# Performance work log

Hardware: AMD Instinct MI355X
Metric: run time of the kernel (lower is better)

## Reference

```python
import jax, jax.numpy as jnp
import numpy as np

B, C_IN, H, W = 4, 128, 56, 56
G = 4            # num_groups
K = 3            # kernel_size
PAD = 1
STRIDE = 1
NG = 8           # grid_size (num RBF centers)
GRID_MIN, GRID_MAX = -1.0, 1.0
C_OUT = 128
CG = C_IN // G           # 32 channels per group
D = CG * K * K           # 288 per-group patch dim
OG = C_OUT // G          # 32 outputs per group


def setup_inputs() -> dict:
    key = jax.random.key(0)
    k1, k2, k3, k4 = jax.random.split(key, 4)
    x = jax.random.normal(k1, (B, C_IN, H, W), dtype=jnp.float32)
    spline_w = jax.random.normal(k2, (G, OG, D * NG), dtype=jnp.float32) * (1.0 / np.sqrt(D * NG))
    base_w = jax.random.normal(k3, (G, OG, D), dtype=jnp.float32) * (1.0 / np.sqrt(D))
    base_b = jax.random.normal(k4, (G, OG), dtype=jnp.float32) * 0.01
    return {"x": x, "spline_w": spline_w, "base_w": base_w, "base_b": base_b}


def _im2col(x):
    # x: (B, C, H, W) -> patches (B, C*K*K, Ho, Wo), unfold ordering (c, kh, kw)
    xp = jnp.pad(x, ((0, 0), (0, 0), (PAD, PAD), (PAD, PAD)))
    Ho = (H + 2 * PAD - K) // STRIDE + 1
    Wo = (W + 2 * PAD - K) // STRIDE + 1
    # fixed 3x3 loop over kernel offsets (9 slices), vectorized over B,C,H,W
    shards = [xp[:, :, i:i + Ho, j:j + Wo] for i in range(K) for j in range(K)]
    p = jnp.stack(shards, axis=2)             # (B, C, K*K, Ho, Wo)
    return p.reshape(x.shape[0], -1, Ho, Wo)  # (B, C*K*K, Ho, Wo)


def reference(x, spline_w, base_w, base_b):
    Ho = (H + 2 * PAD - K) // STRIDE + 1
    Wo = (W + 2 * PAD - K) // STRIDE + 1
    L = Ho * Wo
    patches = _im2col(x)                                   # (B, C*9, Ho, Wo)
    # groups are contiguous channel blocks -> split channel-major patch dim
    p = patches.reshape(B, G, D, L).transpose(0, 1, 3, 2)  # (B, G, L, D)
    # RBF spline basis: exp(-((x - c)/h)^2)
    grid = jnp.linspace(GRID_MIN, GRID_MAX, NG, dtype=p.dtype)   # (NG,)
    h = (GRID_MAX - GRID_MIN) / (NG - 1)
    basis = jnp.exp(-(((p[..., None] - grid) / h) ** 2))         # (B, G, L, D, NG)
    basis = basis.reshape(B, G, L, D * NG)
    spline_out = jnp.einsum('bgld,god->bglo', basis, spline_w)   # (B, G, L, OG)
    base_out = jnp.einsum('bgld,god->bglo', jax.nn.silu(p), base_w) + base_b[None, :, None, :]
    out = spline_out + base_out                                  # (B, G, L, OG)
    # torch.cat(group outs, dim=1) -> per-pixel channel order is group-major
    out = out.transpose(0, 2, 1, 3).reshape(B, L, G * OG)        # (B, L, C_OUT)
    out = out.transpose(0, 2, 1).reshape(B, C_OUT, Ho, Wo)
    return out
```

## Files before the change

kernel.cpp:

```cpp
#include <hip/hip_runtime.h>

#define BATCH 4
#define C_IN 128
#define HWD 56
#define L_PIX 3136
#define G_GRP 4
#define CG 32
#define D_DIM 288
#define NG 8
#define OG 32
#define NQ_SPL 72
#define NQ_BASE 9
#define LOG2E 1.44269504f

typedef short  short8 __attribute__((ext_vector_type(8)));
typedef float  f32x4  __attribute__((ext_vector_type(4)));

__device__ __forceinline__ short f2bf(float f) {
    __bf16 h = (__bf16)f;
    return __builtin_bit_cast(short, h);
}

__global__ __launch_bounds__(256) void convert_w_kernel(
    const float* __restrict__ spline_w,
    const float* __restrict__ base_w,
    short* __restrict__ wspl,
    short* __restrict__ wbase)
{
    int t = blockIdx.x * 256 + threadIdx.x;
    if (t >= G_GRP * (NQ_SPL + NQ_BASE) * 2 * 64) return;
    int lane = t & 63;
    int rest = t >> 6;
    int ot = rest & 1;
    int gq = rest >> 1;
    int g  = gq / (NQ_SPL + NQ_BASE);
    int q  = gq - g * (NQ_SPL + NQ_BASE);
    int o  = ot * 16 + (lane & 15);
    int dl = lane >> 4;
    if (q < NQ_SPL) {
        int d = 4 * q + dl;
        const float* src = spline_w + (size_t)(g * OG + o) * (D_DIM * NG) + d * NG;
        short* dst = wspl + ((size_t)((g * NQ_SPL + q) * 2 + ot) * 64 + lane) * 8;
#pragma unroll
        for (int j = 0; j < 8; ++j) dst[j] = f2bf(src[j]);
    } else {
        int qb = q - NQ_SPL;
        int d0 = qb * 32 + dl * 8;
        const float* src = base_w + (size_t)(g * OG + o) * D_DIM + d0;
        short* dst = wbase + ((size_t)((g * NQ_BASE + qb) * 2 + ot) * 64 + lane) * 8;
#pragma unroll
        for (int j = 0; j < 8; ++j) dst[j] = f2bf(src[j]);
    }
}

__global__ __launch_bounds__(256, 3) void groupkan_mfma_kernel(
    const float* __restrict__ x,
    const float* __restrict__ base_b,
    const short* __restrict__ wspl,
    const short* __restrict__ wbase,
    float* __restrict__ out)
{
    __shared__ float xt[CG][4][58];

    const int tid  = threadIdx.x;
    const int tile = blockIdx.x;
    const int bg   = blockIdx.y;
    const int b = bg >> 2, g = bg & 3;
    const int l0 = tile * 64;
    const int y0 = l0 / HWD;

    const float* xg = x + (size_t)(b * C_IN + g * CG) * L_PIX;
    for (int e = tid; e < CG * 4 * 58; e += 256) {
        int c  = e / 232;
        int r  = e - c * 232;
        int ry = r / 58;
        int rx = r - ry * 58;
        int y  = y0 - 1 + ry;
        int xc = rx - 1;
        float v = 0.0f;
        if (y >= 0 && y < HWD && xc >= 0 && xc < HWD)
            v = xg[(size_t)c * L_PIX + y * HWD + xc];
        xt[c][ry][rx] = v;
    }
    __syncthreads();

    const int lane = tid & 63;
    const int wid  = tid >> 6;
    const int fr   = lane & 15;
    const int dl   = lane >> 4;
    const int l    = l0 + wid * 16 + fr;
    const int yy   = l / HWD;
    const int xx   = l - yy * HWD;
    const int ybase = yy - y0;

    f32x4 acc0, acc1;
    {
        float b0 = base_b[g * OG + fr];
        float b1 = base_b[g * OG + 16 + fr];
        acc0 = (f32x4){b0, b0, b0, b0};
        acc1 = (f32x4){b1, b1, b1, b1};
    }

    const short8* wspg = (const short8*)wspl + (size_t)g * NQ_SPL * 2 * 64;
    const short8* wbg  = (const short8*)wbase + (size_t)g * NQ_BASE * 2 * 64;

    int c = 0, kk = dl;
    for (int q = 0; q < NQ_SPL; ++q) {
        int kh = (kk * 11) >> 5;
        int kw = kk - kh * 3;
        float v = xt[c][ybase + kh][xx + kw];
        float v35p = v * 3.5f + 3.5f;
        short8 a;
#pragma unroll
        for (int j = 0; j < 8; ++j) {
            float u = v35p - (float)j;
            float e = __builtin_amdgcn_exp2f(u * u * (-LOG2E));
            a[j] = f2bf(e);
        }
        short8 bf0 = wspg[(q * 2 + 0) * 64 + lane];
        short8 bf1 = wspg[(q * 2 + 1) * 64 + lane];
        acc0 = __builtin_amdgcn_mfma_f32_16x16x32_bf16(a, bf0, acc0, 0, 0, 0);
        acc1 = __builtin_amdgcn_mfma_f32_16x16x32_bf16(a, bf1, acc1, 0, 0, 0);
        kk += 4; if (kk >= 9) { kk -= 9; ++c; }
    }

    for (int q = 0; q < NQ_BASE; ++q) {
        int d0 = q * 32 + dl * 8;
        int cc = (d0 * 456) >> 12;
        int kb = d0 - cc * 9;
        short8 a;
#pragma unroll
        for (int j = 0; j < 8; ++j) {
            int kh = (kb * 11) >> 5;
            int kw = kb - kh * 3;
            float v = xt[cc][ybase + kh][xx + kw];
            float ex = __builtin_amdgcn_exp2f(v * (-LOG2E));
            float s  = v * __builtin_amdgcn_rcpf(1.0f + ex);
            a[j] = f2bf(s);
            ++kb; if (kb == 9) { kb = 0; ++cc; }
        }
        short8 bf0 = wbg[(q * 2 + 0) * 64 + lane];
        short8 bf1 = wbg[(q * 2 + 1) * 64 + lane];
        acc0 = __builtin_amdgcn_mfma_f32_16x16x32_bf16(a, bf0, acc0, 0, 0, 0);
        acc1 = __builtin_amdgcn_mfma_f32_16x16x32_bf16(a, bf1, acc1, 0, 0, 0);
    }

    float* outp = out + (size_t)(b * C_IN + g * OG) * L_PIX;
    int pix = l0 + wid * 16 + dl * 4;
    *(f32x4*)(outp + (size_t)fr * L_PIX + pix)        = acc0;
    *(f32x4*)(outp + (size_t)(16 + fr) * L_PIX + pix) = acc1;
}

extern "C" void kernel_launch(void* const* d_in, const int* in_sizes, int n_in,
                              void* d_out, int out_size, void* d_ws, size_t ws_size,
                              hipStream_t stream) {
    const float* x        = (const float*)d_in[0];
    const float* spline_w = (const float*)d_in[1];
    const float* base_w   = (const float*)d_in[2];
    const float* base_b   = (const float*)d_in[3];
    float* out = (float*)d_out;

    short* wspl  = (short*)d_ws;
    short* wbase = wspl + (size_t)G_GRP * NQ_SPL * 2 * 64 * 8;

    int conv_threads = G_GRP * (NQ_SPL + NQ_BASE) * 2 * 64;
    convert_w_kernel<<<(conv_threads + 255) / 256, 256, 0, stream>>>(
        spline_w, base_w, wspl, wbase);

    dim3 grid(L_PIX / 64, BATCH * G_GRP);
    groupkan_mfma_kernel<<<grid, 256, 0, stream>>>(x, base_b, wspl, wbase, out);
}
```

Before: 114.5 us.

## Reassign reduction dim per lane, fold RBF scaling into exp2, vectorize weight conversion

```diff
diff --git a/kernel.cpp b/kernel.cpp
--- a/kernel.cpp
+++ b/kernel.cpp
@@ -12,14 +12,21 @@
 #define NQ_SPL 72
 #define NQ_BASE 9
 #define LOG2E 1.44269504f
+#define SQRT_L 1.2011224087f
+#define A_SCL  4.2039284306f
 
 typedef short  short8 __attribute__((ext_vector_type(8)));
 typedef float  f32x4  __attribute__((ext_vector_type(4)));
-
-__device__ __forceinline__ short f2bf(float f) {
-    __bf16 h = (__bf16)f;
-    return __builtin_bit_cast(short, h);
-}
+typedef unsigned int u32x4 __attribute__((ext_vector_type(4)));
+
+__device__ __forceinline__ unsigned int pack2(float lo, float hi) {
+    unsigned short a = __builtin_bit_cast(unsigned short, (__bf16)lo);
+    unsigned short b = __builtin_bit_cast(unsigned short, (__bf16)hi);
+    return (unsigned int)a | ((unsigned int)b << 16);
+}
+
+#define N_SPL_CHUNK (G_GRP * OG * D_DIM)
+#define N_BASE_CHUNK (G_GRP * OG * D_DIM / 8)
 
 __global__ __launch_bounds__(256) void convert_w_kernel(
     const float* __restrict__ spline_w,
@@ -28,28 +35,42 @@
     short* __restrict__ wbase)
 {
     int t = blockIdx.x * 256 + threadIdx.x;
-    if (t >= G_GRP * (NQ_SPL + NQ_BASE) * 2 * 64) return;
-    int lane = t & 63;
-    int rest = t >> 6;
-    int ot = rest & 1;
-    int gq = rest >> 1;
-    int g  = gq / (NQ_SPL + NQ_BASE);
-    int q  = gq - g * (NQ_SPL + NQ_BASE);
-    int o  = ot * 16 + (lane & 15);
-    int dl = lane >> 4;
-    if (q < NQ_SPL) {
-        int d = 4 * q + dl;
-        const float* src = spline_w + (size_t)(g * OG + o) * (D_DIM * NG) + d * NG;
-        short* dst = wspl + ((size_t)((g * NQ_SPL + q) * 2 + ot) * 64 + lane) * 8;
-#pragma unroll
-        for (int j = 0; j < 8; ++j) dst[j] = f2bf(src[j]);
+    if (t >= N_SPL_CHUNK + N_BASE_CHUNK) return;
+    if (t < N_SPL_CHUNK) {
+        const f32x4* s4 = (const f32x4*)spline_w + (size_t)t * 2;
+        f32x4 lo = s4[0], hi = s4[1];
+        int flat = t * 8;
+        int g = flat / (OG * D_DIM * NG);
+        int r = flat - g * (OG * D_DIM * NG);
+        int o = r / (D_DIM * NG);
+        int d = (r - o * (D_DIM * NG)) >> 3;
+        int dl = d / 72;
+        int q  = d - dl * 72;
+        int lane = dl * 16 + (o & 15);
+        int ot = o >> 4;
+        u32x4 pk;
+        pk.x = pack2(lo.x, lo.y); pk.y = pack2(lo.z, lo.w);
+        pk.z = pack2(hi.x, hi.y); pk.w = pack2(hi.z, hi.w);
+        u32x4* dst = (u32x4*)wspl + (((size_t)(g * NQ_SPL + q) * 2 + ot) * 64 + lane);
+        *dst = pk;
     } else {
-        int qb = q - NQ_SPL;
-        int d0 = qb * 32 + dl * 8;
-        const float* src = base_w + (size_t)(g * OG + o) * D_DIM + d0;
-        short* dst = wbase + ((size_t)((g * NQ_BASE + qb) * 2 + ot) * 64 + lane) * 8;
-#pragma unroll
-        for (int j = 0; j < 8; ++j) dst[j] = f2bf(src[j]);
+        int tb = t - N_SPL_CHUNK;
+        const f32x4* s4 = (const f32x4*)base_w + (size_t)tb * 2;
+        f32x4 lo = s4[0], hi = s4[1];
+        int flat = tb * 8;
+        int g = flat / (OG * D_DIM);
+        int r = flat - g * (OG * D_DIM);
+        int o = r / D_DIM;
+        int d0 = r - o * D_DIM;
+        int dl = d0 / 72;
+        int q  = (d0 - dl * 72) >> 3;
+        int lane = dl * 16 + (o & 15);
+        int ot = o >> 4;
+        u32x4 pk;
+        pk.x = pack2(lo.x, lo.y); pk.y = pack2(lo.z, lo.w);
+        pk.z = pack2(hi.x, hi.y); pk.w = pack2(hi.z, hi.w);
+        u32x4* dst = (u32x4*)wbase + (((size_t)(g * NQ_BASE + q) * 2 + ot) * 64 + lane);
+        *dst = pk;
     }
 }
 
@@ -93,6 +114,8 @@
     const int xx   = l - yy * HWD;
     const int ybase = yy - y0;
 
+    const float* P = (const float*)xt + (dl * 8) * 232 + ybase * 58 + xx;
+
     f32x4 acc0, acc1;
     {
         float b0 = base_b[g * OG + fr];
@@ -101,46 +124,61 @@
         acc1 = (f32x4){b1, b1, b1, b1};
     }
 
-    const short8* wspg = (const short8*)wspl + (size_t)g * NQ_SPL * 2 * 64;
-    const short8* wbg  = (const short8*)wbase + (size_t)g * NQ_BASE * 2 * 64;
-
-    int c = 0, kk = dl;
-    for (int q = 0; q < NQ_SPL; ++q) {
-        int kh = (kk * 11) >> 5;
-        int kw = kk - kh * 3;
-        float v = xt[c][ybase + kh][xx + kw];
-        float v35p = v * 3.5f + 3.5f;
-        short8 a;
+    const short8* wl  = (const short8*)wspl + (size_t)g * NQ_SPL * 2 * 64 + lane;
+    const short8* wbl = (const short8*)wbase + (size_t)g * NQ_BASE * 2 * 64 + lane;
+
+    for (int qo = 0; qo < 8; ++qo) {
+        const float* Pc = P + qo * 232;
+#pragma unroll
+        for (int qi = 0; qi < 9; ++qi) {
+            const int kh = qi / 3, kw = qi % 3;
+            float v  = Pc[kh * 58 + kw];
+            float ap = v * A_SCL + A_SCL;
+            float e0, e1, e2, e3, e4, e5, e6, e7;
+            {
+                float u;
+                u = ap - 0.0f * SQRT_L; e0 = __builtin_amdgcn_exp2f(-(u * u));
+                u = ap - 1.0f * SQRT_L; e1 = __builtin_amdgcn_exp2f(-(u * u));
+                u = ap - 2.0f * SQRT_L; e2 = __builtin_amdgcn_exp2f(-(u * u));
+                u = ap - 3.0f * SQRT_L; e3 = __builtin_amdgcn_exp2f(-(u * u));
+                u = ap - 4.0f * SQRT_L; e4 = __builtin_amdgcn_exp2f(-(u * u));
+                u = ap - 5.0f * SQRT_L; e5 = __builtin_amdgcn_exp2f(-(u * u));
+                u = ap - 6.0f * SQRT_L; e6 = __builtin_amdgcn_exp2f(-(u * u));
+                u = ap - 7.0f * SQRT_L; e7 = __builtin_amdgcn_exp2f(-(u * u));
+            }
+            u32x4 pk;
+            pk.x = pack2(e0, e1); pk.y = pack2(e2, e3);
+            pk.z = pack2(e4, e5); pk.w = pack2(e6, e7);
+            short8 a = __builtin_bit_cast(short8, pk);
+            const int q = qo * 9 + qi;
+            short8 bf0 = wl[(q * 2 + 0) * 64];
+            short8 bf1 = wl[(q * 2 + 1) * 64];
+            acc0 = __builtin_amdgcn_mfma_f32_16x16x32_bf16(a, bf0, acc0, 0, 0, 0);
+            acc1 = __builtin_amdgcn_mfma_f32_16x16x32_bf16(a, bf1, acc1, 0, 0, 0);
+        }
+    }
+
+#pragma unroll
+    for (int q = 0; q < 9; ++q) {
+        float s0, s1, s2, s3, s4, s5, s6, s7;
 #pragma unroll
         for (int j = 0; j < 8; ++j) {
-            float u = v35p - (float)j;
-            float e = __builtin_amdgcn_exp2f(u * u * (-LOG2E));
-            a[j] = f2bf(e);
+            const int dd = 8 * q + j;
+            const int co = dd / 9, kk = dd % 9;
+            const int kh = kk / 3, kw = kk % 3;
+            float v  = P[co * 232 + kh * 58 + kw];
+            float ex = __builtin_amdgcn_exp2f(-(v * LOG2E));
+            float s  = v * __builtin_amdgcn_rcpf(1.0f + ex);
+            if (j == 0) s0 = s; else if (j == 1) s1 = s; else if (j == 2) s2 = s;
+            else if (j == 3) s3 = s; else if (j == 4) s4 = s; else if (j == 5) s5 = s;
+            else if (j == 6) s6 = s; else s7 = s;
         }
-        short8 bf0 = wspg[(q * 2 + 0) * 64 + lane];
-        short8 bf1 = wspg[(q * 2 + 1) * 64 + lane];
-        acc0 = __builtin_amdgcn_mfma_f32_16x16x32_bf16(a, bf0, acc0, 0, 0, 0);
-        acc1 = __builtin_amdgcn_mfma_f32_16x16x32_bf16(a, bf1, acc1, 0, 0, 0);
-        kk += 4; if (kk >= 9) { kk -= 9; ++c; }
-    }
-
-    for (int q = 0; q < NQ_BASE; ++q) {
-        int d0 = q * 32 + dl * 8;
-        int cc = (d0 * 456) >> 12;
-        int kb = d0 - cc * 9;
-        short8 a;
-#pragma unroll
-        for (int j = 0; j < 8; ++j) {
-            int kh = (kb * 11) >> 5;
-            int kw = kb - kh * 3;
-            float v = xt[cc][ybase + kh][xx + kw];
-            float ex = __builtin_amdgcn_exp2f(v * (-LOG2E));
-            float s  = v * __builtin_amdgcn_rcpf(1.0f + ex);
-            a[j] = f2bf(s);
-            ++kb; if (kb == 9) { kb = 0; ++cc; }
-        }
-        short8 bf0 = wbg[(q * 2 + 0) * 64 + lane];
-        short8 bf1 = wbg[(q * 2 + 1) * 64 + lane];
+        u32x4 pk;
+        pk.x = pack2(s0, s1); pk.y = pack2(s2, s3);
+        pk.z = pack2(s4, s5); pk.w = pack2(s6, s7);
+        short8 a = __builtin_bit_cast(short8, pk);
+        short8 bf0 = wbl[(q * 2 + 0) * 64];
+        short8 bf1 = wbl[(q * 2 + 1) * 64];
         acc0 = __builtin_amdgcn_mfma_f32_16x16x32_bf16(a, bf0, acc0, 0, 0, 0);
         acc1 = __builtin_amdgcn_mfma_f32_16x16x32_bf16(a, bf1, acc1, 0, 0, 0);
     }
@@ -163,7 +201,7 @@
     short* wspl  = (short*)d_ws;
     short* wbase = wspl + (size_t)G_GRP * NQ_SPL * 2 * 64 * 8;
 
-    int conv_threads = G_GRP * (NQ_SPL + NQ_BASE) * 2 * 64;
+    int conv_threads = N_SPL_CHUNK + N_BASE_CHUNK;
     convert_w_kernel<<<(conv_threads + 255) / 256, 256, 0, stream>>>(
         spline_w, base_w, wspl, wbase);
 
```

Result: faster. 110.7 us (-3.3%).
